# Kernel tuning notes

Hardware: AMD Instinct MI355X
Metric: run time of the kernel (lower is better)

## Reference

```python
import jax, jax.numpy as jnp
import numpy as np

N = 100000       # nodes
E = 1600000      # edges (avg degree 16)
F_IN = 128       # feats_per_node
F1 = 128         # layer_1_feats
F2 = 128         # layer_2_feats


def setup_inputs() -> dict:
    key = jax.random.key(0)
    k1, k2, k3, k4, k5, k6 = jax.random.split(key, 6)
    node_feats = jax.random.normal(k1, (N, F_IN), dtype=jnp.float32)
    # COO representation of sparse normalized adjacency Ahat
    edge_rows = jax.random.randint(k2, (E,), 0, N)
    edge_cols = jax.random.randint(k3, (E,), 0, N)
    edge_vals = jax.random.uniform(k4, (E,), dtype=jnp.float32)
    # reset_param-style init: uniform in +-1/sqrt(fan_in)
    w0 = jax.random.uniform(k5, (F_IN, F1), dtype=jnp.float32,
                            minval=-1.0, maxval=1.0) / np.sqrt(F_IN)
    w1 = jax.random.uniform(k6, (F1, F2), dtype=jnp.float32,
                            minval=-1.0, maxval=1.0) / np.sqrt(F1)
    return {"node_feats": node_feats, "edge_vals": edge_vals,
            "w0": w0, "w1": w1,
            "edge_rows": edge_rows, "edge_cols": edge_cols}


def _spmm(edge_rows, edge_cols, edge_vals, x):
    # out[i] = sum_{(i,j) in edges} val_ij * x[j]   (Ahat @ x)
    msgs = edge_vals[:, None] * x[edge_cols]          # [E, F] gather
    return jax.ops.segment_sum(msgs, edge_rows, num_segments=N)


def reference(node_feats, edge_vals, w0, w1, edge_rows, edge_cols):
    # layer 0: relu(Ahat @ (X @ W0))
    h = jax.nn.relu(_spmm(edge_rows, edge_cols, edge_vals, node_feats @ w0))
    # layer 1: relu(Ahat @ (H @ W1))
    h = jax.nn.relu(_spmm(edge_rows, edge_cols, edge_vals, h @ w1))
    return h
```

## Files before the change

kernel.cpp:

```cpp
#include <hip/hip_runtime.h>

#define N_NODES 100000
#define N_EDGES 1600000
#define F 128
#define M_PAD 100032

#define BUCKET_BITS 9
#define BUCKET_SIZE 512
#define NBUCKETS 196
#define BCAP 9216
#define EPB_A 8192
#define ABLOCKS 196

#define AS1 __attribute__((address_space(1)))
#define AS3 __attribute__((address_space(3)))

typedef __attribute__((ext_vector_type(8))) short short8;
typedef __attribute__((ext_vector_type(4))) float f32x4;

__device__ __forceinline__ float bf_lo(unsigned int u) { return __uint_as_float(u << 16); }
__device__ __forceinline__ float bf_hi(unsigned int u) { return __uint_as_float(u & 0xffff0000u); }
__device__ __forceinline__ unsigned short f2bf(float f) {
    unsigned int u = __float_as_uint(f);
    u += 0x7fffu + ((u >> 16) & 1u);
    return (unsigned short)(u >> 16);
}
__device__ __forceinline__ void gload_lds16(const void* g, void* l) {
    __builtin_amdgcn_global_load_lds((const AS1 unsigned int*)g, (AS3 unsigned int*)l, 16, 0, 0);
}


__global__ void binit_kernel(int* __restrict__ bucket_cursor) {
    int t = threadIdx.x;
    if (t < NBUCKETS) bucket_cursor[t] = t * BCAP;
}

__global__ __launch_bounds__(256) void binA_kernel(const int* __restrict__ rows,
                                                   const int* __restrict__ cols,
                                                   const float* __restrict__ vals,
                                                   int* __restrict__ bucket_cursor,
                                                   uint2* __restrict__ stage) {
    __shared__ int hist[NBUCKETS];
    __shared__ int base[NBUCKETS];
    int tid = threadIdx.x;
    int start = blockIdx.x * EPB_A;
    int cnt = min(EPB_A, N_EDGES - start);
    for (int i = tid; i < NBUCKETS; i += 256) hist[i] = 0;
    __syncthreads();
    for (int i = tid; i < cnt; i += 256) atomicAdd(&hist[rows[start + i] >> BUCKET_BITS], 1);
    __syncthreads();
    for (int i = tid; i < NBUCKETS; i += 256) {
        int h = hist[i];
        base[i] = h ? atomicAdd(&bucket_cursor[i], h) : 0;
        hist[i] = 0;
    }
    __syncthreads();
    for (int i = tid; i < cnt; i += 256) {
        int r = rows[start + i];
        int c = cols[start + i];
        unsigned vb = __float_as_uint(vals[start + i]);
        int b = r >> BUCKET_BITS;
        int p = base[b] + atomicAdd(&hist[b], 1);
        stage[p] = make_uint2(((unsigned)(r & (BUCKET_SIZE - 1)) << 17) | (unsigned)c, vb);
    }
}

__global__ __launch_bounds__(1024) void binB_kernel(const uint2* __restrict__ stage,
                                                    const int* __restrict__ bucket_cursor,
                                                    uint2* __restrict__ csr,
                                                    uint2* __restrict__ rowseg) {
    __shared__ int hist[BUCKET_SIZE];
    __shared__ int scanv[BUCKET_SIZE];
    __shared__ int cur[BUCKET_SIZE];
    int b = blockIdx.x;
    int t = threadIdx.x;
    int s0 = b * BCAP;
    int cnt = bucket_cursor[b] - s0;
    if (t < BUCKET_SIZE) hist[t] = 0;
    __syncthreads();
    for (int i = t; i < cnt; i += 1024) atomicAdd(&hist[stage[s0 + i].x >> 17], 1);
    __syncthreads();
    if (t < BUCKET_SIZE) scanv[t] = hist[t];
    __syncthreads();
    for (int off = 1; off < BUCKET_SIZE; off <<= 1) {
        int x = 0;
        if (t < BUCKET_SIZE && t >= off) x = scanv[t - off];
        __syncthreads();
        if (t < BUCKET_SIZE) scanv[t] += x;
        __syncthreads();
    }
    if (t < BUCKET_SIZE) {
        int st = s0 + scanv[t] - hist[t];
        cur[t] = st;
        int row = (b << BUCKET_BITS) + t;
        if (row < N_NODES) rowseg[row] = make_uint2((unsigned)st, (unsigned)(st + hist[t]));
    }
    __syncthreads();
    for (int i = t; i < cnt; i += 1024) {
        uint2 e = stage[s0 + i];
        int p = atomicAdd(&cur[e.x >> 17], 1);
        csr[p] = make_uint2(e.x & 0x1FFFFu, e.y);
    }
}

__global__ __launch_bounds__(256) void wtrans_kernel(const float* __restrict__ W,
                                                     unsigned short* __restrict__ Wt) {
    int t = threadIdx.x;
    int c = t & 127;
    int o0 = (t >> 7) * 8;
    for (int o = o0; o < o0 + 8; ++o) {
        short8 v;
#pragma unroll
        for (int e = 0; e < 8; ++e) v[e] = (short)f2bf(W[(o * 8 + e) * 128 + c]);
        *(short8*)((char*)Wt + c * 256 + ((o * 16) ^ ((c & 7) << 4))) = v;
    }
}

template <bool IN_BF16>
__global__ __launch_bounds__(256) void mfma_gemm_kernel(const void* __restrict__ Av,
                                                        const unsigned short* __restrict__ Wt,
                                                        unsigned short* __restrict__ T) {
    __shared__ alignas(16) unsigned short wlds[128 * 128];
    __shared__ alignas(16) unsigned short alds[64 * 128];
    int tid = threadIdx.x;
    int w = tid >> 6, l = tid & 63;
    int q = l >> 4, c16 = l & 15;
    long r0 = (long)blockIdx.x * 64;

#pragma unroll
    for (int i = 0; i < 8; ++i) {
        int row = w * 32 + i * 4 + q;
        gload_lds16((const char*)Wt + row * 256 + c16 * 16,
                    (char*)wlds + (w * 8192 + i * 1024));
    }
    if constexpr (IN_BF16) {
#pragma unroll
        for (int i = 0; i < 4; ++i) {
            int row = w * 16 + i * 4 + q;
            gload_lds16((const char*)Av + (r0 + row) * 256 + c16 * 16,
                        (char*)alds + (w * 4096 + i * 1024));
        }
    } else {
        const float* X = (const float*)Av;
#pragma unroll
        for (int i = 0; i < 4; ++i) {
            int row = i * 16 + (tid >> 4);
            int oct = tid & 15;
            long rg = r0 + row;
            if (rg > N_NODES - 1) rg = N_NODES - 1;
            const float4* xp = (const float4*)(X + rg * 128 + oct * 8);
            float4 a = xp[0], bb = xp[1];
            short8 v;
            v[0] = (short)f2bf(a.x); v[1] = (short)f2bf(a.y);
            v[2] = (short)f2bf(a.z); v[3] = (short)f2bf(a.w);
            v[4] = (short)f2bf(bb.x); v[5] = (short)f2bf(bb.y);
            v[6] = (short)f2bf(bb.z); v[7] = (short)f2bf(bb.w);
            *(short8*)((char*)alds + row * 256 + ((oct * 16) ^ ((row & 7) << 4))) = v;
        }
    }
    __syncthreads();

    f32x4 acc[8] = {};
    int nrow = w * 16 + c16;
    int nswz = (nrow & 7) << 4;
#pragma unroll
    for (int ks = 0; ks < 4; ++ks) {
        int kb = ks * 64 + q * 16;
        short8 bfrag = *(const short8*)((const char*)alds + nrow * 256 + (kb ^ nswz));
#pragma unroll
        for (int fb = 0; fb < 8; ++fb) {
            int frow = fb * 16 + c16;
            short8 afrag = *(const short8*)((const char*)wlds + frow * 256 +
                                            (kb ^ ((frow & 7) << 4)));
            acc[fb] = __builtin_amdgcn_mfma_f32_16x16x32_bf16(afrag, bfrag, acc[fb], 0, 0, 0);
        }
    }

    long node = r0 + w * 16 + c16;
#pragma unroll
    for (int fb = 0; fb < 8; ++fb) {
        uint2 o;
        o.x = (unsigned)f2bf(acc[fb][0]) | ((unsigned)f2bf(acc[fb][1]) << 16);
        o.y = (unsigned)f2bf(acc[fb][2]) | ((unsigned)f2bf(acc[fb][3]) << 16);
        *(uint2*)((char*)T + node * 256 + fb * 32 + q * 8) = o;
    }
}

template <bool OUT_BF16>
__global__ __launch_bounds__(256) void spmm_relu_kernel(const uint2* __restrict__ rowseg,
                                                        const uint2* __restrict__ csr,
                                                        const unsigned int* __restrict__ Tu,
                                                        void* __restrict__ outv) {
    int wave = threadIdx.x >> 6;
    int lane = threadIdx.x & 63;
    int row = blockIdx.x * 4 + wave;
    uint2 se = rowseg[row];
    int s = (int)se.x;
    int e = (int)se.y;
    float ax = 0.f, ay = 0.f;
    for (int base = s; base < e; base += 64) {
        int cnt = min(64, e - base);
        int col_l = 0; float val_l = 0.f;
        if (lane < cnt) {
            uint2 ed = csr[base + lane];
            col_l = (int)ed.x;
            val_l = __uint_as_float(ed.y);
        }
        int j = 0;
        for (; j + 8 <= cnt; j += 8) {
            int cc[8]; float vv[8]; unsigned xx[8];
#pragma unroll
            for (int i = 0; i < 8; ++i) {
                cc[i] = __shfl(col_l, j + i);
                vv[i] = __shfl(val_l, j + i);
            }
#pragma unroll
            for (int i = 0; i < 8; ++i) xx[i] = Tu[cc[i] * 64 + lane];
#pragma unroll
            for (int i = 0; i < 8; ++i) {
                ax = fmaf(vv[i], bf_lo(xx[i]), ax);
                ay = fmaf(vv[i], bf_hi(xx[i]), ay);
            }
        }
        for (; j + 2 <= cnt; j += 2) {
            int   c0 = __shfl(col_l, j),     c1 = __shfl(col_l, j + 1);
            float v0 = __shfl(val_l, j),     v1 = __shfl(val_l, j + 1);
            unsigned x0 = Tu[c0 * 64 + lane];
            unsigned x1 = Tu[c1 * 64 + lane];
            ax = fmaf(v0, bf_lo(x0), ax); ay = fmaf(v0, bf_hi(x0), ay);
            ax = fmaf(v1, bf_lo(x1), ax); ay = fmaf(v1, bf_hi(x1), ay);
        }
        for (; j < cnt; ++j) {
            int   c = __shfl(col_l, j);
            float v = __shfl(val_l, j);
            unsigned x = Tu[c * 64 + lane];
            ax = fmaf(v, bf_lo(x), ax); ay = fmaf(v, bf_hi(x), ay);
        }
    }
    ax = fmaxf(ax, 0.f);
    ay = fmaxf(ay, 0.f);
    if constexpr (OUT_BF16) {
        unsigned int* o = (unsigned int*)outv;
        o[row * 64 + (lane ^ ((row & 7) << 2))] =
            (unsigned int)f2bf(ax) | ((unsigned int)f2bf(ay) << 16);
    } else {
        float2* o = (float2*)((float*)outv + row * 128 + lane * 2);
        *o = make_float2(ax, ay);
    }
}

extern "C" void kernel_launch(void* const* d_in, const int* in_sizes, int n_in,
                              void* d_out, int out_size, void* d_ws, size_t ws_size,
                              hipStream_t stream) {
    const float* X     = (const float*)d_in[0];
    const float* evals = (const float*)d_in[1];
    const float* W0    = (const float*)d_in[2];
    const float* W1    = (const float*)d_in[3];
    const int* erows   = (const int*)d_in[4];
    const int* ecols   = (const int*)d_in[5];
    float* out = (float*)d_out;

    char* ws = (char*)d_ws;
    size_t off = 0;
    auto carve = [&](size_t bytes) {
        char* p = ws + off;
        off += (bytes + 255) & ~(size_t)255;
        return p;
    };
    unsigned short* T   = (unsigned short*)carve((size_t)M_PAD * F * 2);
    unsigned short* H   = (unsigned short*)carve((size_t)M_PAD * F * 2);
    unsigned short* Wt0 = (unsigned short*)carve(128 * 128 * 2);
    unsigned short* Wt1 = (unsigned short*)carve(128 * 128 * 2);
    uint2* stage        = (uint2*)carve((size_t)NBUCKETS * BCAP * 8);
    uint2* csr          = (uint2*)carve((size_t)NBUCKETS * BCAP * 8);
    uint2* rowseg       = (uint2*)carve((size_t)N_NODES * 8);
    int* bucket_cursor  = (int*)carve((size_t)NBUCKETS * 4);
    (void)ws_size; (void)in_sizes; (void)n_in; (void)out_size;

    wtrans_kernel<<<1, 256, 0, stream>>>(W0, Wt0);
    wtrans_kernel<<<1, 256, 0, stream>>>(W1, Wt1);

    binit_kernel<<<1, 256, 0, stream>>>(bucket_cursor);
    binA_kernel<<<ABLOCKS, 256, 0, stream>>>(erows, ecols, evals, bucket_cursor, stage);
    binB_kernel<<<NBUCKETS, 1024, 0, stream>>>(stage, bucket_cursor, csr, rowseg);

    int gemm_grid = M_PAD / 64;

    mfma_gemm_kernel<false><<<gemm_grid, 256, 0, stream>>>(X, Wt0, T);
    spmm_relu_kernel<true><<<N_NODES / 4, 256, 0, stream>>>(rowseg, csr,
                                                            (const unsigned int*)T, H);

    mfma_gemm_kernel<true><<<gemm_grid, 256, 0, stream>>>(H, Wt1, T);
    spmm_relu_kernel<false><<<N_NODES / 4, 256, 0, stream>>>(rowseg, csr,
                                                             (const unsigned int*)T, out);
}
```

Before: 202.4 us.

## Split SpMM wave into half-waves gathering two edges per load, merge prep launches

The SpMM kernel now has each half-wave process alternate edges, with each lane loading 8 bytes (four bf16 features) instead of 4. The two halves are reduced with a cross-half shuffle before ReLU and store. The CSR buffer gets zero-padding per bucket and a tail, so padded lanes read harmless zero-weight entries and the remainder loops can go. The weight transposes and cursor init are merged into one launch, and binB's block scan becomes a wave-shuffle scan to cut barriers.

```diff
diff --git a/kernel.cpp b/kernel.cpp
--- a/kernel.cpp
+++ b/kernel.cpp
@@ -29,11 +29,30 @@
     __builtin_amdgcn_global_load_lds((const AS1 unsigned int*)g, (AS3 unsigned int*)l, 16, 0, 0);
 }
 
-
-__global__ void binit_kernel(int* __restrict__ bucket_cursor) {
+__global__ __launch_bounds__(256) void prep_kernel(const float* __restrict__ W0,
+                                                   const float* __restrict__ W1,
+                                                   unsigned short* __restrict__ Wt0,
+                                                   unsigned short* __restrict__ Wt1,
+                                                   int* __restrict__ bucket_cursor,
+                                                   uint2* __restrict__ csr_tail) {
     int t = threadIdx.x;
-    if (t < NBUCKETS) bucket_cursor[t] = t * BCAP;
-}
+    if (blockIdx.x == 2) {
+        if (t < NBUCKETS) bucket_cursor[t] = t * BCAP;
+        if (t >= 192 && t < 256) csr_tail[t - 192] = make_uint2(0u, 0u);
+        return;
+    }
+    const float* W = (blockIdx.x == 0) ? W0 : W1;
+    unsigned short* Wt = (blockIdx.x == 0) ? Wt0 : Wt1;
+    int c = t & 127;
+    int o0 = (t >> 7) * 8;
+    for (int o = o0; o < o0 + 8; ++o) {
+        short8 v;
+#pragma unroll
+        for (int e = 0; e < 8; ++e) v[e] = (short)f2bf(W[(o * 8 + e) * 128 + c]);
+        *(short8*)((char*)Wt + c * 256 + ((o * 16) ^ ((c & 7) << 4))) = v;
+    }
+}
+
 
 __global__ __launch_bounds__(256) void binA_kernel(const int* __restrict__ rows,
                                                    const int* __restrict__ cols,
@@ -72,6 +91,7 @@
     __shared__ int hist[BUCKET_SIZE];
     __shared__ int scanv[BUCKET_SIZE];
     __shared__ int cur[BUCKET_SIZE];
+    __shared__ int wsum[8], woff[8];
     int b = blockIdx.x;
     int t = threadIdx.x;
     int s0 = b * BCAP;
@@ -80,39 +100,37 @@
     __syncthreads();
     for (int i = t; i < cnt; i += 1024) atomicAdd(&hist[stage[s0 + i].x >> 17], 1);
     __syncthreads();
-    if (t < BUCKET_SIZE) scanv[t] = hist[t];
-    __syncthreads();
-    for (int off = 1; off < BUCKET_SIZE; off <<= 1) {
-        int x = 0;
-        if (t < BUCKET_SIZE && t >= off) x = scanv[t - off];
-        __syncthreads();
-        if (t < BUCKET_SIZE) scanv[t] += x;
-        __syncthreads();
-    }
+    int wid = t >> 6, ln = t & 63;
+    if (wid < 8) {
+        int v = hist[wid * 64 + ln];
+#pragma unroll
+        for (int d = 1; d < 64; d <<= 1) {
+            int u = __shfl_up(v, d);
+            if (ln >= d) v += u;
+        }
+        if (ln == 63) wsum[wid] = v;
+        scanv[wid * 64 + ln] = v;
+    }
+    __syncthreads();
+    if (t == 0) {
+        int run = 0;
+#pragma unroll
+        for (int i = 0; i < 8; ++i) { woff[i] = run; run += wsum[i]; }
+    }
+    __syncthreads();
     if (t < BUCKET_SIZE) {
-        int st = s0 + scanv[t] - hist[t];
+        int incl = scanv[t] + woff[t >> 6];
+        int st = s0 + incl - hist[t];
         cur[t] = st;
         int row = (b << BUCKET_BITS) + t;
         if (row < N_NODES) rowseg[row] = make_uint2((unsigned)st, (unsigned)(st + hist[t]));
     }
+    for (int p = s0 + cnt + t; p < s0 + BCAP; p += 1024) csr[p] = make_uint2(0u, 0u);
     __syncthreads();
     for (int i = t; i < cnt; i += 1024) {
         uint2 e = stage[s0 + i];
         int p = atomicAdd(&cur[e.x >> 17], 1);
         csr[p] = make_uint2(e.x & 0x1FFFFu, e.y);
-    }
-}
-
-__global__ __launch_bounds__(256) void wtrans_kernel(const float* __restrict__ W,
-                                                     unsigned short* __restrict__ Wt) {
-    int t = threadIdx.x;
-    int c = t & 127;
-    int o0 = (t >> 7) * 8;
-    for (int o = o0; o < o0 + 8; ++o) {
-        short8 v;
-#pragma unroll
-        for (int e = 0; e < 8; ++e) v[e] = (short)f2bf(W[(o * 8 + e) * 128 + c]);
-        *(short8*)((char*)Wt + c * 256 + ((o * 16) ^ ((c & 7) << 4))) = v;
     }
 }
 
@@ -189,63 +207,57 @@
 template <bool OUT_BF16>
 __global__ __launch_bounds__(256) void spmm_relu_kernel(const uint2* __restrict__ rowseg,
                                                         const uint2* __restrict__ csr,
-                                                        const unsigned int* __restrict__ Tu,
+                                                        const uint2* __restrict__ T2,
                                                         void* __restrict__ outv) {
     int wave = threadIdx.x >> 6;
     int lane = threadIdx.x & 63;
+    int half = lane >> 5;
+    int fl = lane & 31;
     int row = blockIdx.x * 4 + wave;
     uint2 se = rowseg[row];
-    int s = (int)se.x;
-    int e = (int)se.y;
-    float ax = 0.f, ay = 0.f;
+    int s = (int)se.x, e = (int)se.y;
+    float a0 = 0.f, a1 = 0.f, a2 = 0.f, a3 = 0.f;
     for (int base = s; base < e; base += 64) {
         int cnt = min(64, e - base);
-        int col_l = 0; float val_l = 0.f;
-        if (lane < cnt) {
-            uint2 ed = csr[base + lane];
-            col_l = (int)ed.x;
-            val_l = __uint_as_float(ed.y);
-        }
-        int j = 0;
-        for (; j + 8 <= cnt; j += 8) {
-            int cc[8]; float vv[8]; unsigned xx[8];
-#pragma unroll
-            for (int i = 0; i < 8; ++i) {
-                cc[i] = __shfl(col_l, j + i);
-                vv[i] = __shfl(val_l, j + i);
+        uint2 ed = csr[base + lane];
+        int col_l = (lane < cnt) ? (int)ed.x : 0;
+        float val_l = (lane < cnt) ? __uint_as_float(ed.y) : 0.f;
+        int rounds = (cnt + 7) >> 3;
+        for (int r = 0; r < rounds; ++r) {
+            int j = r * 8;
+            int cc[4]; float vv[4]; uint2 xx[4];
+#pragma unroll
+            for (int i = 0; i < 4; ++i) {
+                cc[i] = __shfl(col_l, j + 2 * i + half);
+                vv[i] = __shfl(val_l, j + 2 * i + half);
             }
 #pragma unroll
-            for (int i = 0; i < 8; ++i) xx[i] = Tu[cc[i] * 64 + lane];
-#pragma unroll
-            for (int i = 0; i < 8; ++i) {
-                ax = fmaf(vv[i], bf_lo(xx[i]), ax);
-                ay = fmaf(vv[i], bf_hi(xx[i]), ay);
+            for (int i = 0; i < 4; ++i) xx[i] = T2[cc[i] * 32 + fl];
+#pragma unroll
+            for (int i = 0; i < 4; ++i) {
+                a0 = fmaf(vv[i], bf_lo(xx[i].x), a0);
+                a1 = fmaf(vv[i], bf_hi(xx[i].x), a1);
+                a2 = fmaf(vv[i], bf_lo(xx[i].y), a2);
+                a3 = fmaf(vv[i], bf_hi(xx[i].y), a3);
             }
         }
-        for (; j + 2 <= cnt; j += 2) {
-            int   c0 = __shfl(col_l, j),     c1 = __shfl(col_l, j + 1);
-            float v0 = __shfl(val_l, j),     v1 = __shfl(val_l, j + 1);
-            unsigned x0 = Tu[c0 * 64 + lane];
-            unsigned x1 = Tu[c1 * 64 + lane];
-            ax = fmaf(v0, bf_lo(x0), ax); ay = fmaf(v0, bf_hi(x0), ay);
-            ax = fmaf(v1, bf_lo(x1), ax); ay = fmaf(v1, bf_hi(x1), ay);
-        }
-        for (; j < cnt; ++j) {
-            int   c = __shfl(col_l, j);
-            float v = __shfl(val_l, j);
-            unsigned x = Tu[c * 64 + lane];
-            ax = fmaf(v, bf_lo(x), ax); ay = fmaf(v, bf_hi(x), ay);
-        }
-    }
-    ax = fmaxf(ax, 0.f);
-    ay = fmaxf(ay, 0.f);
-    if constexpr (OUT_BF16) {
-        unsigned int* o = (unsigned int*)outv;
-        o[row * 64 + (lane ^ ((row & 7) << 2))] =
-            (unsigned int)f2bf(ax) | ((unsigned int)f2bf(ay) << 16);
-    } else {
-        float2* o = (float2*)((float*)outv + row * 128 + lane * 2);
-        *o = make_float2(ax, ay);
+    }
+    a0 += __shfl_xor(a0, 32);
+    a1 += __shfl_xor(a1, 32);
+    a2 += __shfl_xor(a2, 32);
+    a3 += __shfl_xor(a3, 32);
+    if (half == 0) {
+        a0 = fmaxf(a0, 0.f); a1 = fmaxf(a1, 0.f);
+        a2 = fmaxf(a2, 0.f); a3 = fmaxf(a3, 0.f);
+        if constexpr (OUT_BF16) {
+            uint2 o;
+            o.x = (unsigned)f2bf(a0) | ((unsigned)f2bf(a1) << 16);
+            o.y = (unsigned)f2bf(a2) | ((unsigned)f2bf(a3) << 16);
+            *(uint2*)((char*)outv + (size_t)row * 256 + ((fl * 8) ^ ((row & 7) << 4))) = o;
+        } else {
+            *(float4*)((float*)outv + (size_t)row * 128 + fl * 4) =
+                make_float4(a0, a1, a2, a3);
+        }
     }
 }
 
@@ -272,15 +284,15 @@
     unsigned short* Wt0 = (unsigned short*)carve(128 * 128 * 2);
     unsigned short* Wt1 = (unsigned short*)carve(128 * 128 * 2);
     uint2* stage        = (uint2*)carve((size_t)NBUCKETS * BCAP * 8);
-    uint2* csr          = (uint2*)carve((size_t)NBUCKETS * BCAP * 8);
+    uint2* csr          = (uint2*)carve(((size_t)NBUCKETS * BCAP + 64) * 8);
     uint2* rowseg       = (uint2*)carve((size_t)N_NODES * 8);
     int* bucket_cursor  = (int*)carve((size_t)NBUCKETS * 4);
     (void)ws_size; (void)in_sizes; (void)n_in; (void)out_size;
 
-    wtrans_kernel<<<1, 256, 0, stream>>>(W0, Wt0);
-    wtrans_kernel<<<1, 256, 0, stream>>>(W1, Wt1);
-
-    binit_kernel<<<1, 256, 0, stream>>>(bucket_cursor);
+    uint2* csr_tail = csr + (size_t)NBUCKETS * BCAP;
+
+    prep_kernel<<<3, 256, 0, stream>>>(W0, W1, Wt0, Wt1, bucket_cursor, csr_tail);
+
     binA_kernel<<<ABLOCKS, 256, 0, stream>>>(erows, ecols, evals, bucket_cursor, stage);
     binB_kernel<<<NBUCKETS, 1024, 0, stream>>>(stage, bucket_cursor, csr, rowseg);
 
@@ -288,9 +300,9 @@
 
     mfma_gemm_kernel<false><<<gemm_grid, 256, 0, stream>>>(X, Wt0, T);
     spmm_relu_kernel<true><<<N_NODES / 4, 256, 0, stream>>>(rowseg, csr,
-                                                            (const unsigned int*)T, H);
+                                                            (const uint2*)T, H);
 
     mfma_gemm_kernel<true><<<gemm_grid, 256, 0, stream>>>(H, Wt1, T);
     spmm_relu_kernel<false><<<N_NODES / 4, 256, 0, stream>>>(rowseg, csr,
-                                                             (const unsigned int*)T, out);
-}
+                                                             (const uint2*)T, out);
+}
```

New measurement: 195.9 us. 3.2% less time.
